# Optimization experiments

Hardware: AMD Instinct MI355X
Metric: run time of the kernel (lower is better)

Reference implementation:

```python
import jax, jax.numpy as jnp
import numpy as np

N, F, D = 50000, 64, 3
E = 800000
H = 128          # local MLP hidden / output dim
G = 256          # global MLP output dim


def _init_linear(key, fan_in, fan_out):
    kw, kb = jax.random.split(key)
    W = jax.random.normal(kw, (fan_in, fan_out), dtype=jnp.float32) / np.sqrt(fan_in)
    b = jax.random.normal(kb, (fan_out,), dtype=jnp.float32) * 0.01
    return W, b


def setup_inputs() -> dict:
    key = jax.random.key(0)
    kx, kp, ke, k1, k2, kg = jax.random.split(key, 6)
    x = jax.random.normal(kx, (N, F), dtype=jnp.float32)
    pos = jax.random.uniform(kp, (N, D), dtype=jnp.float32)
    edge_index = jax.random.randint(ke, (2, E), 0, N, dtype=jnp.int64)
    W1, b1 = _init_linear(k1, F + D, H)   # local_nn layer 1
    W2, b2 = _init_linear(k2, H, H)       # local_nn layer 2
    Wg, bg = _init_linear(kg, H, G)       # global_nn
    return {"x": x, "pos": pos, "W1": W1, "b1": b1, "W2": W2, "b2": b2,
            "Wg": Wg, "bg": bg, "edge_index": edge_index}


def reference(x, pos, W1, b1, W2, b2, Wg, bg, edge_index):
    n = x.shape[0]
    # add self loops (duplicate edges are harmless under max-reduction)
    loops = jnp.arange(n, dtype=edge_index.dtype)
    ei = jnp.concatenate([edge_index, jnp.stack([loops, loops])], axis=1)
    row, col = ei[0], ei[1]            # row = target i, col = neighbor j
    rel = pos[col] - pos[row]          # [E+N, D]
    h = jnp.concatenate([x[col], rel], axis=1)          # [E+N, F+D]
    h = jax.nn.relu(h @ W1 + b1)                         # local MLP
    h = jax.nn.relu(h @ W2 + b2)                         # [E+N, H]
    agg = jax.ops.segment_max(h, row, num_segments=n)    # scatter-max per node
    out = jax.nn.relu(agg @ Wg + bg)                      # global MLP [N, G]
    return out
```

## Files before the change

### kernel.cpp

```cpp
#include <hip/hip_runtime.h>
#include <hip/hip_bf16.h>

typedef __attribute__((ext_vector_type(4))) float f32x4;
typedef __attribute__((ext_vector_type(8))) short bf16x8;

#define EDGE_GRID 1536
#define OUT_GRID  1024

__device__ __forceinline__ unsigned int packbf(float lo, float hi) {
    __hip_bfloat16 l = __float2bfloat16(lo), h = __float2bfloat16(hi);
    const unsigned short lu = *reinterpret_cast<unsigned short*>(&l);
    const unsigned short hu = *reinterpret_cast<unsigned short*>(&h);
    return (unsigned int)lu | ((unsigned int)hu << 16);
}
__device__ __forceinline__ unsigned short bf1(float f) {
    __hip_bfloat16 v = __float2bfloat16(f);
    return *reinterpret_cast<unsigned short*>(&v);
}

__global__ __launch_bounds__(256) void prep_kernel(
    const float* __restrict__ x, const float* __restrict__ W1,
    const float* __restrict__ b1, const float* __restrict__ W2,
    const float* __restrict__ Wg, const int* __restrict__ ei,
    unsigned short* __restrict__ u, unsigned short* __restrict__ W2t,
    unsigned short* __restrict__ Wgt, int* __restrict__ deg,
    int N, int E, int nTot, int NB_U, int NB_C)
{
    __shared__ float sx[8][64];
    const int blk = blockIdx.x;
    const int t = threadIdx.x;
    if (blk < NB_U) {
        const int base = blk * 8;
        for (int i = t; i < 512; i += 256) {
            const int node = base + (i >> 6);
            sx[i >> 6][i & 63] = (node < N) ? x[(size_t)node * 64 + (i & 63)] : 0.0f;
        }
        __syncthreads();
        const int half = t >> 7, col = t & 127;
        const float bias = b1[col];
        float acc[4] = {bias, bias, bias, bias};
#pragma unroll 8
        for (int k = 0; k < 64; ++k) {
            const float w = W1[k * 128 + col];
#pragma unroll
            for (int j = 0; j < 4; ++j)
                acc[j] = fmaf(sx[half * 4 + j][k], w, acc[j]);
        }
#pragma unroll
        for (int j = 0; j < 4; ++j) {
            const int node = base + half * 4 + j;
            if (node < N) u[(size_t)node * 128 + col] = bf1(acc[j]);
        }
    } else if (blk < NB_U + NB_C) {
        const int i = (blk - NB_U) * 256 + t;
        if (i < nTot) {
            const int row = (i < E) ? ei[i] : i - E;
            atomicAdd(deg + row, 1);
        }
    } else {
        const int i = (blk - NB_U - NB_C) * 256 + t;
        if (i < 16384) {
            const int n = i >> 7, k = i & 127;
            W2t[i] = bf1(W2[k * 128 + n]);
        } else if (i < 49152) {
            const int j = i - 16384;
            const int n = j >> 7, k = j & 127;
            Wgt[j] = bf1(Wg[k * 256 + n]);
        }
    }
}

__global__ __launch_bounds__(1024) void scan_kernel(
    const int* __restrict__ deg, int* __restrict__ offs, int N)
{
    __shared__ int sc[1024];
    const int t = threadIdx.x;
    const int c0 = t * 52;
    int v[52];
    int s = 0;
#pragma unroll
    for (int j4 = 0; j4 < 13; ++j4) {
        const int idx = c0 + j4 * 4;
        int4 d = {0, 0, 0, 0};
        if (idx + 3 < N) d = *(const int4*)(deg + idx);
        else {
            if (idx     < N) d.x = deg[idx];
            if (idx + 1 < N) d.y = deg[idx + 1];
            if (idx + 2 < N) d.z = deg[idx + 2];
        }
        v[j4*4+0] = s; s += d.x;
        v[j4*4+1] = s; s += d.y;
        v[j4*4+2] = s; s += d.z;
        v[j4*4+3] = s; s += d.w;
    }
    sc[t] = s;
    __syncthreads();
    for (int off = 1; off < 1024; off <<= 1) {
        const int val = (t >= off) ? sc[t - off] : 0;
        __syncthreads();
        sc[t] += val;
        __syncthreads();
    }
    const int base = sc[t] - s;
#pragma unroll
    for (int j4 = 0; j4 < 13; ++j4) {
        const int idx = c0 + j4 * 4;
        const int4 o = {base + v[j4*4], base + v[j4*4+1], base + v[j4*4+2], base + v[j4*4+3]};
        if (idx + 3 < N) *(int4*)(offs + idx) = o;
        else {
            if (idx     < N) offs[idx]     = o.x;
            if (idx + 1 < N) offs[idx + 1] = o.y;
            if (idx + 2 < N) offs[idx + 2] = o.z;
        }
    }
}

__global__ void scatter_kernel(const int* __restrict__ ei, const int* __restrict__ offs,
                               int* __restrict__ deg, int* __restrict__ srow,
                               int* __restrict__ scol, int E, int nTot)
{
    const int i = blockIdx.x * 256 + threadIdx.x;
    if (i < nTot) {
        int row, col;
        if (i < E) { row = ei[i]; col = ei[E + i]; }
        else       { row = col = i - E; }
        const int p = atomicSub(deg + row, 1) - 1;
        const int q = offs[row] + p;
        srow[q] = row;
        scol[q] = col;
    }
}

__global__ __launch_bounds__(256, 6) void edge_kernel(
    const unsigned short* __restrict__ u, const float* __restrict__ pos,
    const float* __restrict__ W1, const float* __restrict__ b2,
    const unsigned short* __restrict__ W2t, const int* __restrict__ srow,
    const int* __restrict__ scol, unsigned int* __restrict__ agg,
    int nTot, int nTiles)
{
    __shared__ unsigned short sh1[4096];
    __shared__ float          sh2[4096];
    __shared__ float          sW1p[480];
    __shared__ int            sRowL[2][32];

    const int t = threadIdx.x;
    const int wv = t >> 6, lane = t & 63;
    const int m = lane & 15, g = lane >> 4;
    const int n0 = wv * 32 + m;
    const int e_h1 = t >> 3, s8 = t & 7, kc = s8 * 16;
    const int wb = s8 * 18;
    const int cR = t & 127, hR = t >> 7;

    bf16x8 bfr[2][4];
#pragma unroll
    for (int nb = 0; nb < 2; ++nb)
#pragma unroll
        for (int ks = 0; ks < 4; ++ks)
            bfr[nb][ks] = *(const bf16x8*)(W2t + (size_t)(n0 + nb * 16) * 128 + (ks * 4 + g) * 8);
    const float bia0 = b2[n0], bia1 = b2[n0 + 16];

    for (int i = t; i < 384; i += 256) {
        const int r = i >> 7, k = i & 127;
        sW1p[r * 160 + k + 2 * (k >> 4)] = W1[64 * 128 + i];
    }
    __syncthreads();

    auto gather = [&](int tile, int& c, float& r0, float& r1, float& r2,
                      uint4& ua, uint4& ub, int& rowStage) {
        c = -1; rowStage = -1;
        if (tile < nTiles) {
            const int p = tile * 32 + e_h1;
            if (p < nTot) {
                c = scol[p];
                const int r = srow[p];
                r0 = pos[c * 3 + 0] - pos[r * 3 + 0];
                r1 = pos[c * 3 + 1] - pos[r * 3 + 1];
                r2 = pos[c * 3 + 2] - pos[r * 3 + 2];
                const uint4* up = (const uint4*)(u + (size_t)c * 128 + kc);
                ua = up[0]; ub = up[1];
            }
            if (t < 32) {
                const int p2 = tile * 32 + t;
                rowStage = (p2 < nTot) ? srow[p2] : -1;
            }
        }
    };
    auto computeH1 = [&](int buf, int c, float r0, float r1, float r2,
                         uint4 ua, uint4 ub, int rowStage) {
        unsigned int ow[8] = {0,0,0,0,0,0,0,0};
        if (c >= 0) {
            const unsigned int uw[8] = {ua.x, ua.y, ua.z, ua.w, ub.x, ub.y, ub.z, ub.w};
#pragma unroll
            for (int j = 0; j < 8; ++j) {
                const int wk = wb + 2 * j;
                float lo = __uint_as_float(uw[j] << 16);
                float hi = __uint_as_float(uw[j] & 0xFFFF0000u);
                lo = fmaf(r0, sW1p[wk],       fmaf(r1, sW1p[160 + wk],     fmaf(r2, sW1p[320 + wk],     lo)));
                hi = fmaf(r0, sW1p[wk + 1],   fmaf(r1, sW1p[160 + wk + 1], fmaf(r2, sW1p[320 + wk + 1], hi)));
                ow[j] = packbf(fmaxf(lo, 0.0f), fmaxf(hi, 0.0f));
            }
        }
        const int g0 = e_h1 * 16 + s8 * 2;
        ((int4*)sh1)[(g0)     ^ (e_h1 & 7)] = make_int4(ow[0], ow[1], ow[2], ow[3]);
        ((int4*)sh1)[(g0 + 1) ^ (e_h1 & 7)] = make_int4(ow[4], ow[5], ow[6], ow[7]);
        if (t < 32) sRowL[buf][t] = rowStage;
    };

    {
        int c, rs; float r0 = 0, r1 = 0, r2 = 0; uint4 ua = {0,0,0,0}, ub = {0,0,0,0};
        gather(blockIdx.x, c, r0, r1, r2, ua, ub, rs);
        computeH1(0, c, r0, r1, r2, ua, ub, rs);
    }
    __syncthreads();

    int b = 0;
    for (int tile = blockIdx.x; tile < nTiles; tile += EDGE_GRID, b ^= 1) {
        const int nextTile = tile + EDGE_GRID;

        int c, rs; float r0 = 0, r1 = 0, r2 = 0; uint4 ua = {0,0,0,0}, ub = {0,0,0,0};
        gather(nextTile, c, r0, r1, r2, ua, ub, rs);

        {
            f32x4 acc0 = {0,0,0,0}, acc1 = {0,0,0,0}, acc2 = {0,0,0,0}, acc3 = {0,0,0,0};
#pragma unroll
            for (int ks = 0; ks < 4; ++ks) {
                const int slot = ks * 4 + g;
                const bf16x8 a0 = *(const bf16x8*)&sh1[(m        * 16 + (slot ^ (m & 7))) << 3];
                const bf16x8 a1 = *(const bf16x8*)&sh1[((m + 16) * 16 + (slot ^ (m & 7))) << 3];
                acc0 = __builtin_amdgcn_mfma_f32_16x16x32_bf16(a0, bfr[0][ks], acc0, 0, 0, 0);
                acc1 = __builtin_amdgcn_mfma_f32_16x16x32_bf16(a0, bfr[1][ks], acc1, 0, 0, 0);
                acc2 = __builtin_amdgcn_mfma_f32_16x16x32_bf16(a1, bfr[0][ks], acc2, 0, 0, 0);
                acc3 = __builtin_amdgcn_mfma_f32_16x16x32_bf16(a1, bfr[1][ks], acc3, 0, 0, 0);
            }
#pragma unroll
            for (int rg = 0; rg < 4; ++rg) {
                const int e0 = g * 4 + rg, e1 = 16 + g * 4 + rg;
                sh2[e0 * 128 + ((n0      + e0 * 4) & 127)] = fmaxf(acc0[rg] + bia0, 0.0f);
                sh2[e0 * 128 + ((n0 + 16 + e0 * 4) & 127)] = fmaxf(acc1[rg] + bia1, 0.0f);
                sh2[e1 * 128 + ((n0      + e1 * 4) & 127)] = fmaxf(acc2[rg] + bia0, 0.0f);
                sh2[e1 * 128 + ((n0 + 16 + e1 * 4) & 127)] = fmaxf(acc3[rg] + bia1, 0.0f);
            }
        }
        __syncthreads();

        if (nextTile < nTiles)
            computeH1(b ^ 1, c, r0, r1, r2, ua, ub, rs);

        {
            float run = 0.0f; int cur = -1;
            const int ebase = hR * 16;
            for (int i = 0; i < 16; ++i) {
                const int e = ebase + i;
                const int r = sRowL[b][e];
                if (r < 0) break;
                const float v = sh2[e * 128 + ((cR + e * 4) & 127)];
                if (r != cur) {
                    if (cur >= 0) {
                        const unsigned int bits = __float_as_uint(run);
                        unsigned int* dst = agg + (size_t)cur * 128 + cR;
                        if (bits > *dst) atomicMax(dst, bits);
                    }
                    cur = r; run = v;
                } else run = fmaxf(run, v);
            }
            if (cur >= 0) {
                const unsigned int bits = __float_as_uint(run);
                unsigned int* dst = agg + (size_t)cur * 128 + cR;
                if (bits > *dst) atomicMax(dst, bits);
            }
        }
        __syncthreads();
    }
}

__global__ __launch_bounds__(256, 4) void out_kernel(
    const float* __restrict__ agg, const unsigned short* __restrict__ Wgt,
    const float* __restrict__ bg, float* __restrict__ out, int N, int nTiles)
{
    __shared__ unsigned short sA[4096];

    const int t = threadIdx.x;
    const int wv = t >> 6, lane = t & 63;
    const int m = lane & 15, g = lane >> 4;
    const int eA = t >> 3, kcA = (t & 7) * 16;

    bf16x8 wfr[4][4];
    float bgv[4];
#pragma unroll
    for (int nt = 0; nt < 4; ++nt) {
        const int n = wv * 64 + nt * 16 + m;
#pragma unroll
        for (int ks = 0; ks < 4; ++ks)
            wfr[nt][ks] = *(const bf16x8*)(Wgt + (size_t)n * 128 + (ks * 4 + g) * 8);
        bgv[nt] = bg[n];
    }

    for (int tile = blockIdx.x; tile < nTiles; tile += OUT_GRID) {
        const int tbase = tile * 32;

        {
            unsigned int ow[8] = {0,0,0,0,0,0,0,0};
            const int node = tbase + eA;
            if (node < N) {
                const float4* ap = (const float4*)(agg + (size_t)node * 128 + kcA);
#pragma unroll
                for (int j = 0; j < 4; ++j) {
                    const float4 v = ap[j];
                    ow[j * 2 + 0] = packbf(v.x, v.y);
                    ow[j * 2 + 1] = packbf(v.z, v.w);
                }
            }
            const int g0 = eA * 16 + (t & 7) * 2;
            ((int4*)sA)[(g0)     ^ (eA & 7)] = make_int4(ow[0], ow[1], ow[2], ow[3]);
            ((int4*)sA)[(g0 + 1) ^ (eA & 7)] = make_int4(ow[4], ow[5], ow[6], ow[7]);
        }
        __syncthreads();

        f32x4 acc[2][4] = {{{0,0,0,0},{0,0,0,0},{0,0,0,0},{0,0,0,0}},
                           {{0,0,0,0},{0,0,0,0},{0,0,0,0},{0,0,0,0}}};
#pragma unroll
        for (int ks = 0; ks < 4; ++ks) {
            const int slot = ks * 4 + g;
            const bf16x8 a0 = *(const bf16x8*)&sA[(m        * 16 + (slot ^ (m & 7))) << 3];
            const bf16x8 a1 = *(const bf16x8*)&sA[((m + 16) * 16 + (slot ^ (m & 7))) << 3];
#pragma unroll
            for (int nt = 0; nt < 4; ++nt) {
                acc[0][nt] = __builtin_amdgcn_mfma_f32_16x16x32_bf16(a0, wfr[nt][ks], acc[0][nt], 0, 0, 0);
                acc[1][nt] = __builtin_amdgcn_mfma_f32_16x16x32_bf16(a1, wfr[nt][ks], acc[1][nt], 0, 0, 0);
            }
        }
#pragma unroll
        for (int mg = 0; mg < 2; ++mg)
#pragma unroll
        for (int nt = 0; nt < 4; ++nt) {
            const int n = wv * 64 + nt * 16 + m;
#pragma unroll
            for (int rg = 0; rg < 4; ++rg) {
                const int node = tbase + mg * 16 + g * 4 + rg;
                if (node < N)
                    out[(size_t)node * 256 + n] = fmaxf(acc[mg][nt][rg] + bgv[nt], 0.0f);
            }
        }
        __syncthreads();
    }
}

extern "C" void kernel_launch(void* const* d_in, const int* in_sizes, int n_in,
                              void* d_out, int out_size, void* d_ws, size_t ws_size,
                              hipStream_t stream)
{
    const float* x   = (const float*)d_in[0];
    const float* pos = (const float*)d_in[1];
    const float* W1  = (const float*)d_in[2];
    const float* b1  = (const float*)d_in[3];
    const float* W2  = (const float*)d_in[4];
    const float* b2  = (const float*)d_in[5];
    const float* Wg  = (const float*)d_in[6];
    const float* bg  = (const float*)d_in[7];
    const int*   ei  = (const int*)d_in[8];
    float* out = (float*)d_out;

    const int N    = in_sizes[1] / 3;
    const int E    = in_sizes[8] / 2;
    const int nTot = E + N;

    size_t off = 0;
    auto alloc = [&](size_t bytes) -> void* {
        void* p = (char*)d_ws + off;
        off += (bytes + 255) & ~(size_t)255;
        return p;
    };
    unsigned short* u    = (unsigned short*)alloc((size_t)N * 128 * 2);
    unsigned int*   agg  = (unsigned int*)  alloc((size_t)N * 128 * 4);
    int*            deg  = (int*)           alloc((size_t)N * 4);
    int*            offs = (int*)           alloc((size_t)N * 4);
    int*            srow = (int*)           alloc((size_t)nTot * 4);
    int*            scol = (int*)           alloc((size_t)nTot * 4);
    unsigned short* W2t  = (unsigned short*)alloc(16384 * 2);
    unsigned short* Wgt  = (unsigned short*)alloc(32768 * 2);

    hipMemsetAsync(agg, 0, (size_t)N * 128 * 4, stream);
    hipMemsetAsync(deg, 0, (size_t)N * 4, stream);

    const int NB_U = (N + 7) / 8;
    const int NB_C = (nTot + 255) / 256;
    const int NB_T = 192;
    hipLaunchKernelGGL(prep_kernel, dim3(NB_U + NB_C + NB_T), dim3(256), 0, stream,
                       x, W1, b1, W2, Wg, ei, u, W2t, Wgt, deg, N, E, nTot, NB_U, NB_C);

    hipLaunchKernelGGL(scan_kernel, dim3(1), dim3(1024), 0, stream, deg, offs, N);

    hipLaunchKernelGGL(scatter_kernel, dim3((nTot + 255) / 256), dim3(256), 0, stream,
                       ei, offs, deg, srow, scol, E, nTot);

    const int nTilesE = (nTot + 31) / 32;
    hipLaunchKernelGGL(edge_kernel, dim3(EDGE_GRID), dim3(256), 0, stream,
                       u, pos, W1, b2, W2t, srow, scol, agg, nTot, nTilesE);

    const int nTilesO = (N + 31) / 32;
    hipLaunchKernelGGL(out_kernel, dim3(OUT_GRID), dim3(256), 0, stream,
                       (const float*)agg, Wgt, bg, out, N, nTilesO);
}
```

Measured before the change: 442.0 us.

## Compute first MLP layer per edge with MFMA from bf16 x instead of precomputed u

Drops the per-node precompute of x@W1+b1 (a 128-wide bf16 table). The edge kernel now gathers 64-wide bf16 x rows and runs the first layer as MFMA per edge tile, adding the position term and bias in the epilogue. Row and column indices are packed into one int2 array, the layer-2 output is staged as bf16 in shared memory, one barrier per tile is removed, and grid and occupancy bounds are raised. This halves the gather bytes per edge and removes the prep GEMM, at the cost of extra per-edge MFMA work and bf16 rounding of the inputs and the layer-2 output.

```diff
diff --git a/kernel.cpp b/kernel.cpp
--- a/kernel.cpp
+++ b/kernel.cpp
@@ -4,7 +4,7 @@
 typedef __attribute__((ext_vector_type(4))) float f32x4;
 typedef __attribute__((ext_vector_type(8))) short bf16x8;
 
-#define EDGE_GRID 1536
+#define EDGE_GRID 1792
 #define OUT_GRID  1024
 
 __device__ __forceinline__ unsigned int packbf(float lo, float hi) {
@@ -20,52 +20,36 @@
 
 __global__ __launch_bounds__(256) void prep_kernel(
     const float* __restrict__ x, const float* __restrict__ W1,
-    const float* __restrict__ b1, const float* __restrict__ W2,
-    const float* __restrict__ Wg, const int* __restrict__ ei,
-    unsigned short* __restrict__ u, unsigned short* __restrict__ W2t,
-    unsigned short* __restrict__ Wgt, int* __restrict__ deg,
-    int N, int E, int nTot, int NB_U, int NB_C)
-{
-    __shared__ float sx[8][64];
-    const int blk = blockIdx.x;
-    const int t = threadIdx.x;
-    if (blk < NB_U) {
-        const int base = blk * 8;
-        for (int i = t; i < 512; i += 256) {
-            const int node = base + (i >> 6);
-            sx[i >> 6][i & 63] = (node < N) ? x[(size_t)node * 64 + (i & 63)] : 0.0f;
-        }
-        __syncthreads();
-        const int half = t >> 7, col = t & 127;
-        const float bias = b1[col];
-        float acc[4] = {bias, bias, bias, bias};
-#pragma unroll 8
-        for (int k = 0; k < 64; ++k) {
-            const float w = W1[k * 128 + col];
-#pragma unroll
-            for (int j = 0; j < 4; ++j)
-                acc[j] = fmaf(sx[half * 4 + j][k], w, acc[j]);
-        }
-#pragma unroll
-        for (int j = 0; j < 4; ++j) {
-            const int node = base + half * 4 + j;
-            if (node < N) u[(size_t)node * 128 + col] = bf1(acc[j]);
-        }
-    } else if (blk < NB_U + NB_C) {
-        const int i = (blk - NB_U) * 256 + t;
-        if (i < nTot) {
-            const int row = (i < E) ? ei[i] : i - E;
-            atomicAdd(deg + row, 1);
-        }
+    const float* __restrict__ W2, const float* __restrict__ Wg,
+    const int* __restrict__ ei, unsigned short* __restrict__ xbf,
+    unsigned short* __restrict__ W2t, unsigned short* __restrict__ Wgt,
+    unsigned short* __restrict__ W1at, int* __restrict__ deg,
+    int N64, int E, int nTot, int NB_X, int NB_C)
+{
+    const int blk = blockIdx.x, t = threadIdx.x;
+    if (blk < NB_X) {
+        const int idx = blk * 2048 + t * 8;
+        if (idx < N64) {
+            const float4 f0 = *(const float4*)(x + idx);
+            const float4 f1 = *(const float4*)(x + idx + 4);
+            int4 o;
+            o.x = (int)packbf(f0.x, f0.y); o.y = (int)packbf(f0.z, f0.w);
+            o.z = (int)packbf(f1.x, f1.y); o.w = (int)packbf(f1.z, f1.w);
+            *(int4*)(xbf + idx) = o;
+        }
+    } else if (blk < NB_X + NB_C) {
+        const int i = (blk - NB_X) * 256 + t;
+        if (i < nTot) atomicAdd(deg + ((i < E) ? ei[i] : i - E), 1);
     } else {
-        const int i = (blk - NB_U - NB_C) * 256 + t;
+        const int i = (blk - NB_X - NB_C) * 256 + t;
         if (i < 16384) {
-            const int n = i >> 7, k = i & 127;
-            W2t[i] = bf1(W2[k * 128 + n]);
+            W2t[i] = bf1(W2[(i & 127) * 128 + (i >> 7)]);
         } else if (i < 49152) {
             const int j = i - 16384;
-            const int n = j >> 7, k = j & 127;
-            Wgt[j] = bf1(Wg[k * 256 + n]);
+            Wgt[j] = bf1(Wg[(j & 127) * 256 + (j >> 7)]);
+        } else if (i < 57344) {
+            const int j = i - 49152;
+            W1at[j] = bf1(W1[(j & 63) * 128 + (j >> 6)]);
         }
     }
 }
@@ -116,8 +100,8 @@
 }
 
 __global__ void scatter_kernel(const int* __restrict__ ei, const int* __restrict__ offs,
-                               int* __restrict__ deg, int* __restrict__ srow,
-                               int* __restrict__ scol, int E, int nTot)
+                               int* __restrict__ deg, int2* __restrict__ spair,
+                               int E, int nTot)
 {
     const int i = blockIdx.x * 256 + threadIdx.x;
     if (i < nTot) {
@@ -125,126 +109,140 @@
         if (i < E) { row = ei[i]; col = ei[E + i]; }
         else       { row = col = i - E; }
         const int p = atomicSub(deg + row, 1) - 1;
-        const int q = offs[row] + p;
-        srow[q] = row;
-        scol[q] = col;
-    }
-}
-
-__global__ __launch_bounds__(256, 6) void edge_kernel(
-    const unsigned short* __restrict__ u, const float* __restrict__ pos,
-    const float* __restrict__ W1, const float* __restrict__ b2,
-    const unsigned short* __restrict__ W2t, const int* __restrict__ srow,
-    const int* __restrict__ scol, unsigned int* __restrict__ agg,
-    int nTot, int nTiles)
-{
-    __shared__ unsigned short sh1[4096];
-    __shared__ float          sh2[4096];
-    __shared__ float          sW1p[480];
-    __shared__ int            sRowL[2][32];
+        spair[offs[row] + p] = make_int2(row, col);
+    }
+}
+
+__global__ __launch_bounds__(256, 7) void edge_kernel(
+    const unsigned short* __restrict__ xbf, const float* __restrict__ pos,
+    const float* __restrict__ W1, const float* __restrict__ b1,
+    const float* __restrict__ b2, const unsigned short* __restrict__ W2t,
+    const unsigned short* __restrict__ W1at, const int2* __restrict__ spair,
+    unsigned int* __restrict__ agg, int nTot, int nTiles)
+{
+    __shared__ unsigned short sx1[2048];
+    __shared__ unsigned short sh1b[4096];
+    __shared__ unsigned short sh2u[4096];
+    __shared__ float4 sRel4[32];
+    __shared__ int sRowL[2][32];
 
     const int t = threadIdx.x;
     const int wv = t >> 6, lane = t & 63;
     const int m = lane & 15, g = lane >> 4;
     const int n0 = wv * 32 + m;
-    const int e_h1 = t >> 3, s8 = t & 7, kc = s8 * 16;
-    const int wb = s8 * 18;
+    const int e8 = t >> 3, j8 = t & 7;
     const int cR = t & 127, hR = t >> 7;
 
-    bf16x8 bfr[2][4];
-#pragma unroll
-    for (int nb = 0; nb < 2; ++nb)
+    bf16x8 bfrW2[2][4], bfrA[2][2];
+    float w1pv[2][3], b1v[2], b2v[2];
+#pragma unroll
+    for (int nb = 0; nb < 2; ++nb) {
+        const int n = n0 + nb * 16;
 #pragma unroll
         for (int ks = 0; ks < 4; ++ks)
-            bfr[nb][ks] = *(const bf16x8*)(W2t + (size_t)(n0 + nb * 16) * 128 + (ks * 4 + g) * 8);
-    const float bia0 = b2[n0], bia1 = b2[n0 + 16];
-
-    for (int i = t; i < 384; i += 256) {
-        const int r = i >> 7, k = i & 127;
-        sW1p[r * 160 + k + 2 * (k >> 4)] = W1[64 * 128 + i];
-    }
-    __syncthreads();
-
-    auto gather = [&](int tile, int& c, float& r0, float& r1, float& r2,
-                      uint4& ua, uint4& ub, int& rowStage) {
-        c = -1; rowStage = -1;
+            bfrW2[nb][ks] = *(const bf16x8*)(W2t + (size_t)n * 128 + (ks * 4 + g) * 8);
+#pragma unroll
+        for (int ks = 0; ks < 2; ++ks)
+            bfrA[nb][ks] = *(const bf16x8*)(W1at + (size_t)n * 64 + (ks * 4 + g) * 8);
+#pragma unroll
+        for (int ax = 0; ax < 3; ++ax)
+            w1pv[nb][ax] = W1[(64 + ax) * 128 + n];
+        b1v[nb] = b1[n];
+        b2v[nb] = b2[n];
+    }
+
+    auto gatherX = [&](int tile, uint4& xa, float& r0, float& r1, float& r2, int& rowStage) {
+        xa = make_uint4(0, 0, 0, 0); r0 = r1 = r2 = 0.0f; rowStage = -1;
         if (tile < nTiles) {
-            const int p = tile * 32 + e_h1;
+            const int p = tile * 32 + e8;
             if (p < nTot) {
-                c = scol[p];
-                const int r = srow[p];
-                r0 = pos[c * 3 + 0] - pos[r * 3 + 0];
-                r1 = pos[c * 3 + 1] - pos[r * 3 + 1];
-                r2 = pos[c * 3 + 2] - pos[r * 3 + 2];
-                const uint4* up = (const uint4*)(u + (size_t)c * 128 + kc);
-                ua = up[0]; ub = up[1];
+                const int2 pr = spair[p];
+                xa = *(const uint4*)(xbf + (size_t)pr.y * 64 + j8 * 8);
+                if (j8 == 0) {
+                    r0 = pos[pr.y * 3 + 0] - pos[pr.x * 3 + 0];
+                    r1 = pos[pr.y * 3 + 1] - pos[pr.x * 3 + 1];
+                    r2 = pos[pr.y * 3 + 2] - pos[pr.x * 3 + 2];
+                }
             }
             if (t < 32) {
                 const int p2 = tile * 32 + t;
-                rowStage = (p2 < nTot) ? srow[p2] : -1;
+                rowStage = (p2 < nTot) ? spair[p2].x : -1;
             }
         }
     };
-    auto computeH1 = [&](int buf, int c, float r0, float r1, float r2,
-                         uint4 ua, uint4 ub, int rowStage) {
-        unsigned int ow[8] = {0,0,0,0,0,0,0,0};
-        if (c >= 0) {
-            const unsigned int uw[8] = {ua.x, ua.y, ua.z, ua.w, ub.x, ub.y, ub.z, ub.w};
-#pragma unroll
-            for (int j = 0; j < 8; ++j) {
-                const int wk = wb + 2 * j;
-                float lo = __uint_as_float(uw[j] << 16);
-                float hi = __uint_as_float(uw[j] & 0xFFFF0000u);
-                lo = fmaf(r0, sW1p[wk],       fmaf(r1, sW1p[160 + wk],     fmaf(r2, sW1p[320 + wk],     lo)));
-                hi = fmaf(r0, sW1p[wk + 1],   fmaf(r1, sW1p[160 + wk + 1], fmaf(r2, sW1p[320 + wk + 1], hi)));
-                ow[j] = packbf(fmaxf(lo, 0.0f), fmaxf(hi, 0.0f));
-            }
-        }
-        const int g0 = e_h1 * 16 + s8 * 2;
-        ((int4*)sh1)[(g0)     ^ (e_h1 & 7)] = make_int4(ow[0], ow[1], ow[2], ow[3]);
-        ((int4*)sh1)[(g0 + 1) ^ (e_h1 & 7)] = make_int4(ow[4], ow[5], ow[6], ow[7]);
+    auto stage = [&](int buf, const uint4& xa, float r0, float r1, float r2, int rowStage) {
+        ((uint4*)sx1)[e8 * 8 + (j8 ^ (e8 & 7))] = xa;
+        if (j8 == 0) sRel4[e8] = make_float4(r0, r1, r2, 0.0f);
         if (t < 32) sRowL[buf][t] = rowStage;
     };
 
     {
-        int c, rs; float r0 = 0, r1 = 0, r2 = 0; uint4 ua = {0,0,0,0}, ub = {0,0,0,0};
-        gather(blockIdx.x, c, r0, r1, r2, ua, ub, rs);
-        computeH1(0, c, r0, r1, r2, ua, ub, rs);
+        uint4 xa; float r0, r1, r2; int rs;
+        gatherX(blockIdx.x, xa, r0, r1, r2, rs);
+        stage(0, xa, r0, r1, r2, rs);
     }
     __syncthreads();
 
     int b = 0;
     for (int tile = blockIdx.x; tile < nTiles; tile += EDGE_GRID, b ^= 1) {
-        const int nextTile = tile + EDGE_GRID;
-
-        int c, rs; float r0 = 0, r1 = 0, r2 = 0; uint4 ua = {0,0,0,0}, ub = {0,0,0,0};
-        gather(nextTile, c, r0, r1, r2, ua, ub, rs);
+        uint4 xa; float r0, r1, r2; int rs;
+        gatherX(tile + EDGE_GRID, xa, r0, r1, r2, rs);
+
+        f32x4 h1a[2][2] = {{{0,0,0,0},{0,0,0,0}}, {{0,0,0,0},{0,0,0,0}}};
+#pragma unroll
+        for (int ks = 0; ks < 2; ++ks) {
+            const int slot = ks * 4 + g;
+            const bf16x8 a0 = *(const bf16x8*)&sx1[(m        * 8 + (slot ^ (m & 7))) << 3];
+            const bf16x8 a1 = *(const bf16x8*)&sx1[((m + 16) * 8 + (slot ^ (m & 7))) << 3];
+            h1a[0][0] = __builtin_amdgcn_mfma_f32_16x16x32_bf16(a0, bfrA[0][ks], h1a[0][0], 0, 0, 0);
+            h1a[0][1] = __builtin_amdgcn_mfma_f32_16x16x32_bf16(a0, bfrA[1][ks], h1a[0][1], 0, 0, 0);
+            h1a[1][0] = __builtin_amdgcn_mfma_f32_16x16x32_bf16(a1, bfrA[0][ks], h1a[1][0], 0, 0, 0);
+            h1a[1][1] = __builtin_amdgcn_mfma_f32_16x16x32_bf16(a1, bfrA[1][ks], h1a[1][1], 0, 0, 0);
+        }
+#pragma unroll
+        for (int hf = 0; hf < 2; ++hf)
+#pragma unroll
+        for (int rg = 0; rg < 4; ++rg) {
+            const int e = hf * 16 + g * 4 + rg;
+            const float4 rv = sRel4[e];
+#pragma unroll
+            for (int nb = 0; nb < 2; ++nb) {
+                float h = h1a[hf][nb][rg] + rv.x * w1pv[nb][0] + rv.y * w1pv[nb][1]
+                        + rv.z * w1pv[nb][2] + b1v[nb];
+                h = fmaxf(h, 0.0f);
+                const int hcol = n0 + nb * 16;
+                sh1b[((e * 16 + ((hcol >> 3) ^ (e & 7))) << 3) + (hcol & 7)] = bf1(h);
+            }
+        }
+        __syncthreads();
 
         {
-            f32x4 acc0 = {0,0,0,0}, acc1 = {0,0,0,0}, acc2 = {0,0,0,0}, acc3 = {0,0,0,0};
+            f32x4 acc[2][2] = {{{0,0,0,0},{0,0,0,0}}, {{0,0,0,0},{0,0,0,0}}};
 #pragma unroll
             for (int ks = 0; ks < 4; ++ks) {
                 const int slot = ks * 4 + g;
-                const bf16x8 a0 = *(const bf16x8*)&sh1[(m        * 16 + (slot ^ (m & 7))) << 3];
-                const bf16x8 a1 = *(const bf16x8*)&sh1[((m + 16) * 16 + (slot ^ (m & 7))) << 3];
-                acc0 = __builtin_amdgcn_mfma_f32_16x16x32_bf16(a0, bfr[0][ks], acc0, 0, 0, 0);
-                acc1 = __builtin_amdgcn_mfma_f32_16x16x32_bf16(a0, bfr[1][ks], acc1, 0, 0, 0);
-                acc2 = __builtin_amdgcn_mfma_f32_16x16x32_bf16(a1, bfr[0][ks], acc2, 0, 0, 0);
-                acc3 = __builtin_amdgcn_mfma_f32_16x16x32_bf16(a1, bfr[1][ks], acc3, 0, 0, 0);
-            }
+                const bf16x8 a0 = *(const bf16x8*)&sh1b[(m        * 16 + (slot ^ (m & 7))) << 3];
+                const bf16x8 a1 = *(const bf16x8*)&sh1b[((m + 16) * 16 + (slot ^ (m & 7))) << 3];
+                acc[0][0] = __builtin_amdgcn_mfma_f32_16x16x32_bf16(a0, bfrW2[0][ks], acc[0][0], 0, 0, 0);
+                acc[0][1] = __builtin_amdgcn_mfma_f32_16x16x32_bf16(a0, bfrW2[1][ks], acc[0][1], 0, 0, 0);
+                acc[1][0] = __builtin_amdgcn_mfma_f32_16x16x32_bf16(a1, bfrW2[0][ks], acc[1][0], 0, 0, 0);
+                acc[1][1] = __builtin_amdgcn_mfma_f32_16x16x32_bf16(a1, bfrW2[1][ks], acc[1][1], 0, 0, 0);
+            }
+#pragma unroll
+            for (int hf = 0; hf < 2; ++hf)
 #pragma unroll
             for (int rg = 0; rg < 4; ++rg) {
-                const int e0 = g * 4 + rg, e1 = 16 + g * 4 + rg;
-                sh2[e0 * 128 + ((n0      + e0 * 4) & 127)] = fmaxf(acc0[rg] + bia0, 0.0f);
-                sh2[e0 * 128 + ((n0 + 16 + e0 * 4) & 127)] = fmaxf(acc1[rg] + bia1, 0.0f);
-                sh2[e1 * 128 + ((n0      + e1 * 4) & 127)] = fmaxf(acc2[rg] + bia0, 0.0f);
-                sh2[e1 * 128 + ((n0 + 16 + e1 * 4) & 127)] = fmaxf(acc3[rg] + bia1, 0.0f);
-            }
-        }
-        __syncthreads();
-
-        if (nextTile < nTiles)
-            computeH1(b ^ 1, c, r0, r1, r2, ua, ub, rs);
+                const int e = hf * 16 + g * 4 + rg;
+#pragma unroll
+                for (int nb = 0; nb < 2; ++nb) {
+                    const float v = fmaxf(acc[hf][nb][rg] + b2v[nb], 0.0f);
+                    sh2u[e * 128 + ((n0 + nb * 16 + 2 * e) & 127)] = bf1(v);
+                }
+            }
+        }
+
+        stage(b ^ 1, xa, r0, r1, r2, rs);
+        __syncthreads();
 
         {
             float run = 0.0f; int cur = -1;
@@ -253,7 +251,8 @@
                 const int e = ebase + i;
                 const int r = sRowL[b][e];
                 if (r < 0) break;
-                const float v = sh2[e * 128 + ((cR + e * 4) & 127)];
+                const unsigned short hv = sh2u[e * 128 + ((cR + 2 * e) & 127)];
+                const float v = __uint_as_float((unsigned int)hv << 16);
                 if (r != cur) {
                     if (cur >= 0) {
                         const unsigned int bits = __float_as_uint(run);
@@ -269,7 +268,6 @@
                 if (bits > *dst) atomicMax(dst, bits);
             }
         }
-        __syncthreads();
     }
 }
 
@@ -297,7 +295,6 @@
 
     for (int tile = blockIdx.x; tile < nTiles; tile += OUT_GRID) {
         const int tbase = tile * 32;
-
         {
             unsigned int ow[8] = {0,0,0,0,0,0,0,0};
             const int node = tbase + eA;
@@ -361,6 +358,7 @@
     float* out = (float*)d_out;
 
     const int N    = in_sizes[1] / 3;
+    const int N64  = in_sizes[0];
     const int E    = in_sizes[8] / 2;
     const int nTot = E + N;
 
@@ -370,32 +368,33 @@
         off += (bytes + 255) & ~(size_t)255;
         return p;
     };
-    unsigned short* u    = (unsigned short*)alloc((size_t)N * 128 * 2);
+    unsigned short* xbf  = (unsigned short*)alloc((size_t)N64 * 2);
     unsigned int*   agg  = (unsigned int*)  alloc((size_t)N * 128 * 4);
     int*            deg  = (int*)           alloc((size_t)N * 4);
     int*            offs = (int*)           alloc((size_t)N * 4);
-    int*            srow = (int*)           alloc((size_t)nTot * 4);
-    int*            scol = (int*)           alloc((size_t)nTot * 4);
+    int2*           spair= (int2*)          alloc((size_t)nTot * 8);
     unsigned short* W2t  = (unsigned short*)alloc(16384 * 2);
     unsigned short* Wgt  = (unsigned short*)alloc(32768 * 2);
+    unsigned short* W1at = (unsigned short*)alloc(8192 * 2);
 
     hipMemsetAsync(agg, 0, (size_t)N * 128 * 4, stream);
     hipMemsetAsync(deg, 0, (size_t)N * 4, stream);
 
-    const int NB_U = (N + 7) / 8;
+    const int NB_X = (N64 + 2047) / 2048;
     const int NB_C = (nTot + 255) / 256;
-    const int NB_T = 192;
-    hipLaunchKernelGGL(prep_kernel, dim3(NB_U + NB_C + NB_T), dim3(256), 0, stream,
-                       x, W1, b1, W2, Wg, ei, u, W2t, Wgt, deg, N, E, nTot, NB_U, NB_C);
+    const int NB_T = 224;
+    hipLaunchKernelGGL(prep_kernel, dim3(NB_X + NB_C + NB_T), dim3(256), 0, stream,
+                       x, W1, W2, Wg, ei, xbf, W2t, Wgt, W1at, deg,
+                       N64, E, nTot, NB_X, NB_C);
 
     hipLaunchKernelGGL(scan_kernel, dim3(1), dim3(1024), 0, stream, deg, offs, N);
 
     hipLaunchKernelGGL(scatter_kernel, dim3((nTot + 255) / 256), dim3(256), 0, stream,
-                       ei, offs, deg, srow, scol, E, nTot);
+                       ei, offs, deg, spair, E, nTot);
 
     const int nTilesE = (nTot + 31) / 32;
     hipLaunchKernelGGL(edge_kernel, dim3(EDGE_GRID), dim3(256), 0, stream,
-                       u, pos, W1, b2, W2t, srow, scol, agg, nTot, nTilesE);
+                       xbf, pos, W1, b1, b2, W2t, W1at, spair, agg, nTot, nTilesE);
 
     const int nTilesO = (N + 31) / 32;
     hipLaunchKernelGGL(out_kernel, dim3(OUT_GRID), dim3(256), 0, stream,
```

After: 589.9 us. +33.5%, slower.
